# Kernel optimization log

Measured on AMD Instinct MI355X. Metric: run time of the kernel, lower is better.

Reference implementation:

```python
import jax, jax.numpy as jnp
import numpy as np

N_NODES = 50000
N_EDGES = 1250000
H_FEATS = 64


def setup_inputs() -> dict:
    key = jax.random.key(0)
    k1, k2, k3, k4, k5, k6, k7 = jax.random.split(key, 7)
    h = jax.random.normal(k1, (N_NODES, H_FEATS), dtype=jnp.float32)
    src = jax.random.randint(k2, (N_EDGES,), 0, N_NODES, dtype=jnp.int64)
    dst = jax.random.randint(k3, (N_EDGES,), 0, N_NODES, dtype=jnp.int64)
    # nn.Linear(2*h, h) and nn.Linear(h, 1); store weights as [in, out]
    s1 = 1.0 / np.sqrt(2 * H_FEATS)
    s2 = 1.0 / np.sqrt(H_FEATS)
    W1 = jax.random.uniform(k4, (2 * H_FEATS, H_FEATS), jnp.float32, -s1, s1)
    b1 = jax.random.uniform(k5, (H_FEATS,), jnp.float32, -s1, s1)
    W2 = jax.random.uniform(k6, (H_FEATS, 1), jnp.float32, -s2, s2)
    b2 = jax.random.uniform(k7, (1,), jnp.float32, -s2, s2)
    return {"h": h, "src": src, "dst": dst, "W1": W1, "b1": b1, "W2": W2, "b2": b2}


def reference(h, src, dst, W1, b1, W2, b2):
    # Gather per-edge endpoint features and concat: [E, 2*h_feats]
    he = jnp.concatenate([h[src], h[dst]], axis=1)
    hid = jax.nn.relu(he @ W1 + b1)          # [E, h_feats]
    score = (hid @ W2 + b2)[:, 0]            # [E]
    label = jnp.round(jax.nn.sigmoid(score))  # [E]
    return score, label
```

## Files before the change

kernel.cpp:

```cpp
#include <hip/hip_runtime.h>
#include <hip/hip_bf16.h>

#define H 64
#define NPB 64
#define EPB 128
#define FB_THRESH 0.015f

__device__ __forceinline__ unsigned short f2bf(float f) {
    unsigned u = __float_as_uint(f);
    unsigned r = (u + 0x7fffu + ((u >> 16) & 1u)) >> 16;
    return (unsigned short)r;
}
__device__ __forceinline__ float bf_lo(unsigned w) { return __uint_as_float(w << 16); }
__device__ __forceinline__ float bf_hi(unsigned w) { return __uint_as_float(w & 0xffff0000u); }

__global__ void __launch_bounds__(256)
node_proj_kernel(const float* __restrict__ h,
                 const float* __restrict__ W1,
                 float* __restrict__ A32,
                 float* __restrict__ B32,
                 unsigned short* __restrict__ Abf,
                 unsigned short* __restrict__ Bbf,
                 int n_nodes) {
    __shared__ float sh[NPB * H];
    const int t = threadIdx.x;
    const int c = t & 63;
    const int w = t >> 6;
    const int base = blockIdx.x * NPB;

    {
        const float4* hg = (const float4*)(h + (size_t)base * H);
        float4* shv = (float4*)sh;
#pragma unroll
        for (int i = 0; i < 4; ++i) {
            const int idx = t + i * 256;
            const int node = base + (idx >> 4);
            if (node < n_nodes) shv[idx] = hg[idx];
        }
    }

    float wA[64], wB[64];
#pragma unroll
    for (int k = 0; k < 64; ++k) {
        wA[k] = W1[k * H + c];
        wB[k] = W1[(k + 64) * H + c];
    }
    __syncthreads();

#pragma unroll 1
    for (int n0 = 0; n0 < 8; ++n0) {
        const int nl = w * 16 + n0 * 2;
        const int node = base + nl;
        if (node >= n_nodes) break;
        const bool two = (node + 1) < n_nodes;
        const float4* hr0 = (const float4*)(sh + nl * H);
        const float4* hr1 = (const float4*)(sh + (nl + 1) * H);
        float a0 = 0.f, b0 = 0.f, a1 = 0.f, b1acc = 0.f;
#pragma unroll
        for (int kk = 0; kk < 16; ++kk) {
            const float4 h0 = hr0[kk];
            const float4 h1 = hr1[kk];
            a0 = fmaf(h0.x, wA[4 * kk + 0], a0);
            a0 = fmaf(h0.y, wA[4 * kk + 1], a0);
            a0 = fmaf(h0.z, wA[4 * kk + 2], a0);
            a0 = fmaf(h0.w, wA[4 * kk + 3], a0);
            b0 = fmaf(h0.x, wB[4 * kk + 0], b0);
            b0 = fmaf(h0.y, wB[4 * kk + 1], b0);
            b0 = fmaf(h0.z, wB[4 * kk + 2], b0);
            b0 = fmaf(h0.w, wB[4 * kk + 3], b0);
            a1 = fmaf(h1.x, wA[4 * kk + 0], a1);
            a1 = fmaf(h1.y, wA[4 * kk + 1], a1);
            a1 = fmaf(h1.z, wA[4 * kk + 2], a1);
            a1 = fmaf(h1.w, wA[4 * kk + 3], a1);
            b1acc = fmaf(h1.x, wB[4 * kk + 0], b1acc);
            b1acc = fmaf(h1.y, wB[4 * kk + 1], b1acc);
            b1acc = fmaf(h1.z, wB[4 * kk + 2], b1acc);
            b1acc = fmaf(h1.w, wB[4 * kk + 3], b1acc);
        }
        A32[(size_t)node * H + c] = a0;
        B32[(size_t)node * H + c] = b0;
        Abf[(size_t)node * H + c] = f2bf(a0);
        Bbf[(size_t)node * H + c] = f2bf(b0);
        if (two) {
            A32[(size_t)(node + 1) * H + c] = a1;
            B32[(size_t)(node + 1) * H + c] = b1acc;
            Abf[(size_t)(node + 1) * H + c] = f2bf(a1);
            Bbf[(size_t)(node + 1) * H + c] = f2bf(b1acc);
        }
    }
}

__global__ void __launch_bounds__(256)
edge_score_kernel(const unsigned short* __restrict__ Abf,
                  const unsigned short* __restrict__ Bbf,
                  const float* __restrict__ A32,
                  const float* __restrict__ B32,
                  const int* __restrict__ src,
                  const int* __restrict__ dst,
                  const float* __restrict__ b1,
                  const float* __restrict__ W2,
                  const float* __restrict__ b2,
                  float* __restrict__ score_out,
                  float* __restrict__ label_out,
                  int n_edges) {
    const int t = threadIdx.x;
    const int sub = t & 15;
    const int group = t >> 4;

    const float4 b1v = ((const float4*)b1)[sub];
    const float4 w2v = ((const float4*)W2)[sub];
    const float b2s = b2[0];

    const int e0 = blockIdx.x * EPB + group;

    int ec[8], s[8], d[8];
#pragma unroll
    for (int i = 0; i < 8; ++i) {
        const int e = e0 + i * 16;
        ec[i] = e < n_edges ? e : (n_edges - 1);
    }
#pragma unroll
    for (int i = 0; i < 8; ++i) { s[i] = src[ec[i]]; d[i] = dst[ec[i]]; }

    uint2 av[8], cv[8];
#pragma unroll
    for (int i = 0; i < 8; ++i)
        av[i] = ((const uint2*)(Abf + (size_t)s[i] * H))[sub];
#pragma unroll
    for (int i = 0; i < 8; ++i)
        cv[i] = ((const uint2*)(Bbf + (size_t)d[i] * H))[sub];

#pragma unroll
    for (int i = 0; i < 8; ++i) {
        const float a0 = bf_lo(av[i].x), a1 = bf_hi(av[i].x);
        const float a2 = bf_lo(av[i].y), a3 = bf_hi(av[i].y);
        const float c0 = bf_lo(cv[i].x), c1 = bf_hi(cv[i].x);
        const float c2 = bf_lo(cv[i].y), c3 = bf_hi(cv[i].y);
        const float h0 = fmaxf(a0 + c0 + b1v.x, 0.f);
        const float h1 = fmaxf(a1 + c1 + b1v.y, 0.f);
        const float h2 = fmaxf(a2 + c2 + b1v.z, 0.f);
        const float h3 = fmaxf(a3 + c3 + b1v.w, 0.f);
        float p = h0 * w2v.x + h1 * w2v.y + h2 * w2v.z + h3 * w2v.w;
        p += __shfl_xor(p, 1);
        p += __shfl_xor(p, 2);
        p += __shfl_xor(p, 4);
        p += __shfl_xor(p, 8);
        float sc = p + b2s;

        if (fabsf(sc) < FB_THRESH) {
            const float4 a4 = ((const float4*)(A32 + (size_t)s[i] * H))[sub];
            const float4 c4 = ((const float4*)(B32 + (size_t)d[i] * H))[sub];
            const float g0 = fmaxf(a4.x + c4.x + b1v.x, 0.f);
            const float g1 = fmaxf(a4.y + c4.y + b1v.y, 0.f);
            const float g2 = fmaxf(a4.z + c4.z + b1v.z, 0.f);
            const float g3 = fmaxf(a4.w + c4.w + b1v.w, 0.f);
            float q = g0 * w2v.x + g1 * w2v.y + g2 * w2v.z + g3 * w2v.w;
            q += __shfl_xor(q, 1);
            q += __shfl_xor(q, 2);
            q += __shfl_xor(q, 4);
            q += __shfl_xor(q, 8);
            sc = q + b2s;
        }

        const int e = e0 + i * 16;
        if (sub == 0 && e < n_edges) {
            score_out[e] = sc;
            label_out[e] = sc > 0.f ? 1.f : 0.f;
        }
    }
}

extern "C" void kernel_launch(void* const* d_in, const int* in_sizes, int n_in,
                              void* d_out, int out_size, void* d_ws, size_t ws_size,
                              hipStream_t stream) {
    const float* h   = (const float*)d_in[0];
    const int*   src = (const int*)  d_in[1];
    const int*   dst = (const int*)  d_in[2];
    const float* W1  = (const float*)d_in[3];
    const float* b1  = (const float*)d_in[4];
    const float* W2  = (const float*)d_in[5];
    const float* b2  = (const float*)d_in[6];

    const int n_nodes = in_sizes[0] / H;
    const int n_edges = in_sizes[1];

    float* A32 = (float*)d_ws;
    float* B32 = A32 + (size_t)n_nodes * H;
    unsigned short* Abf = (unsigned short*)(B32 + (size_t)n_nodes * H);
    unsigned short* Bbf = Abf + (size_t)n_nodes * H;

    float* score_out = (float*)d_out;
    float* label_out = score_out + n_edges;

    {
        const int blocks = (n_nodes + NPB - 1) / NPB;
        node_proj_kernel<<<blocks, 256, 0, stream>>>(h, W1, A32, B32, Abf, Bbf,
                                                     n_nodes);
    }
    {
        const int blocks = (n_edges + EPB - 1) / EPB;
        edge_score_kernel<<<blocks, 256, 0, stream>>>(Abf, Bbf, A32, B32,
                                                      src, dst, b1, W2, b2,
                                                      score_out, label_out,
                                                      n_edges);
    }
}
```

Measured before the change: 147.0 us.

## Switch edge gather to fp16 with packed half2 math and 8-lane edge groups

```diff
diff --git a/kernel.cpp b/kernel.cpp
--- a/kernel.cpp
+++ b/kernel.cpp
@@ -3,24 +3,38 @@
 
 #define H 64
 #define NPB 64
-#define EPB 128
-#define FB_THRESH 0.015f
-
-__device__ __forceinline__ unsigned short f2bf(float f) {
-    unsigned u = __float_as_uint(f);
-    unsigned r = (u + 0x7fffu + ((u >> 16) & 1u)) >> 16;
-    return (unsigned short)r;
-}
-__device__ __forceinline__ float bf_lo(unsigned w) { return __uint_as_float(w << 16); }
-__device__ __forceinline__ float bf_hi(unsigned w) { return __uint_as_float(w & 0xffff0000u); }
+#define EPT 8
+#define FB_THRESH 0.008f
+
+typedef _Float16 half2_t __attribute__((ext_vector_type(2)));
+
+__device__ __forceinline__ half2_t h2relu(half2_t x) {
+#if defined(__has_builtin) && __has_builtin(__builtin_elementwise_max)
+    half2_t z = {(_Float16)0.f, (_Float16)0.f};
+    return __builtin_elementwise_max(x, z);
+#else
+    half2_t r;
+    r.x = x.x > (_Float16)0.f ? x.x : (_Float16)0.f;
+    r.y = x.y > (_Float16)0.f ? x.y : (_Float16)0.f;
+    return r;
+#endif
+}
+
+__device__ __forceinline__ float hdot2(half2_t a, half2_t b, float c) {
+#if defined(__has_builtin) && __has_builtin(__builtin_amdgcn_fdot2)
+    return __builtin_amdgcn_fdot2(a, b, c, false);
+#else
+    return c + (float)a.x * (float)b.x + (float)a.y * (float)b.y;
+#endif
+}
 
 __global__ void __launch_bounds__(256)
 node_proj_kernel(const float* __restrict__ h,
                  const float* __restrict__ W1,
                  float* __restrict__ A32,
                  float* __restrict__ B32,
-                 unsigned short* __restrict__ Abf,
-                 unsigned short* __restrict__ Bbf,
+                 _Float16* __restrict__ A16,
+                 _Float16* __restrict__ B16,
                  int n_nodes) {
     __shared__ float sh[NPB * H];
     const int t = threadIdx.x;
@@ -79,20 +93,20 @@
         }
         A32[(size_t)node * H + c] = a0;
         B32[(size_t)node * H + c] = b0;
-        Abf[(size_t)node * H + c] = f2bf(a0);
-        Bbf[(size_t)node * H + c] = f2bf(b0);
+        A16[(size_t)node * H + c] = (_Float16)a0;
+        B16[(size_t)node * H + c] = (_Float16)b0;
         if (two) {
             A32[(size_t)(node + 1) * H + c] = a1;
             B32[(size_t)(node + 1) * H + c] = b1acc;
-            Abf[(size_t)(node + 1) * H + c] = f2bf(a1);
-            Bbf[(size_t)(node + 1) * H + c] = f2bf(b1acc);
+            A16[(size_t)(node + 1) * H + c] = (_Float16)a1;
+            B16[(size_t)(node + 1) * H + c] = (_Float16)b1acc;
         }
     }
 }
 
 __global__ void __launch_bounds__(256)
-edge_score_kernel(const unsigned short* __restrict__ Abf,
-                  const unsigned short* __restrict__ Bbf,
+edge_score_kernel(const _Float16* __restrict__ A16,
+                  const _Float16* __restrict__ B16,
                   const float* __restrict__ A32,
                   const float* __restrict__ B32,
                   const int* __restrict__ src,
@@ -104,65 +118,79 @@
                   float* __restrict__ label_out,
                   int n_edges) {
     const int t = threadIdx.x;
-    const int sub = t & 15;
-    const int group = t >> 4;
-
-    const float4 b1v = ((const float4*)b1)[sub];
-    const float4 w2v = ((const float4*)W2)[sub];
+    const int sub = t & 7;
+    const int group = t >> 3;
+
+    const float4 b1lo = ((const float4*)b1)[sub * 2 + 0];
+    const float4 b1hi = ((const float4*)b1)[sub * 2 + 1];
+    const float4 w2lo = ((const float4*)W2)[sub * 2 + 0];
+    const float4 w2hi = ((const float4*)W2)[sub * 2 + 1];
+    half2_t b1h[4], w2h[4];
+    b1h[0] = (half2_t){(_Float16)b1lo.x, (_Float16)b1lo.y};
+    b1h[1] = (half2_t){(_Float16)b1lo.z, (_Float16)b1lo.w};
+    b1h[2] = (half2_t){(_Float16)b1hi.x, (_Float16)b1hi.y};
+    b1h[3] = (half2_t){(_Float16)b1hi.z, (_Float16)b1hi.w};
+    w2h[0] = (half2_t){(_Float16)w2lo.x, (_Float16)w2lo.y};
+    w2h[1] = (half2_t){(_Float16)w2lo.z, (_Float16)w2lo.w};
+    w2h[2] = (half2_t){(_Float16)w2hi.x, (_Float16)w2hi.y};
+    w2h[3] = (half2_t){(_Float16)w2hi.z, (_Float16)w2hi.w};
     const float b2s = b2[0];
 
-    const int e0 = blockIdx.x * EPB + group;
-
-    int ec[8], s[8], d[8];
-#pragma unroll
-    for (int i = 0; i < 8; ++i) {
-        const int e = e0 + i * 16;
+    const int e0 = blockIdx.x * (256 / 8 * EPT) + group;
+
+    int ec[EPT], s[EPT], d[EPT];
+#pragma unroll
+    for (int i = 0; i < EPT; ++i) {
+        const int e = e0 + i * 32;
         ec[i] = e < n_edges ? e : (n_edges - 1);
     }
 #pragma unroll
-    for (int i = 0; i < 8; ++i) { s[i] = src[ec[i]]; d[i] = dst[ec[i]]; }
-
-    uint2 av[8], cv[8];
-#pragma unroll
-    for (int i = 0; i < 8; ++i)
-        av[i] = ((const uint2*)(Abf + (size_t)s[i] * H))[sub];
-#pragma unroll
-    for (int i = 0; i < 8; ++i)
-        cv[i] = ((const uint2*)(Bbf + (size_t)d[i] * H))[sub];
-
-#pragma unroll
-    for (int i = 0; i < 8; ++i) {
-        const float a0 = bf_lo(av[i].x), a1 = bf_hi(av[i].x);
-        const float a2 = bf_lo(av[i].y), a3 = bf_hi(av[i].y);
-        const float c0 = bf_lo(cv[i].x), c1 = bf_hi(cv[i].x);
-        const float c2 = bf_lo(cv[i].y), c3 = bf_hi(cv[i].y);
-        const float h0 = fmaxf(a0 + c0 + b1v.x, 0.f);
-        const float h1 = fmaxf(a1 + c1 + b1v.y, 0.f);
-        const float h2 = fmaxf(a2 + c2 + b1v.z, 0.f);
-        const float h3 = fmaxf(a3 + c3 + b1v.w, 0.f);
-        float p = h0 * w2v.x + h1 * w2v.y + h2 * w2v.z + h3 * w2v.w;
+    for (int i = 0; i < EPT; ++i) { s[i] = src[ec[i]]; d[i] = dst[ec[i]]; }
+
+    float4 av[EPT], cv[EPT];
+#pragma unroll
+    for (int i = 0; i < EPT; ++i)
+        av[i] = ((const float4*)(A16 + (size_t)s[i] * H))[sub];
+#pragma unroll
+    for (int i = 0; i < EPT; ++i)
+        cv[i] = ((const float4*)(B16 + (size_t)d[i] * H))[sub];
+
+#pragma unroll
+    for (int i = 0; i < EPT; ++i) {
+        const half2_t* a2 = (const half2_t*)&av[i];
+        const half2_t* c2 = (const half2_t*)&cv[i];
+        float p = 0.f;
+#pragma unroll
+        for (int j = 0; j < 4; ++j) {
+            half2_t hj = h2relu(a2[j] + c2[j] + b1h[j]);
+            p = hdot2(hj, w2h[j], p);
+        }
         p += __shfl_xor(p, 1);
         p += __shfl_xor(p, 2);
         p += __shfl_xor(p, 4);
-        p += __shfl_xor(p, 8);
         float sc = p + b2s;
 
         if (fabsf(sc) < FB_THRESH) {
-            const float4 a4 = ((const float4*)(A32 + (size_t)s[i] * H))[sub];
-            const float4 c4 = ((const float4*)(B32 + (size_t)d[i] * H))[sub];
-            const float g0 = fmaxf(a4.x + c4.x + b1v.x, 0.f);
-            const float g1 = fmaxf(a4.y + c4.y + b1v.y, 0.f);
-            const float g2 = fmaxf(a4.z + c4.z + b1v.z, 0.f);
-            const float g3 = fmaxf(a4.w + c4.w + b1v.w, 0.f);
-            float q = g0 * w2v.x + g1 * w2v.y + g2 * w2v.z + g3 * w2v.w;
+            const float4 ra0 = ((const float4*)(A32 + (size_t)s[i] * H))[sub * 2 + 0];
+            const float4 ra1 = ((const float4*)(A32 + (size_t)s[i] * H))[sub * 2 + 1];
+            const float4 rb0 = ((const float4*)(B32 + (size_t)d[i] * H))[sub * 2 + 0];
+            const float4 rb1 = ((const float4*)(B32 + (size_t)d[i] * H))[sub * 2 + 1];
+            float q = 0.f;
+            q += fmaxf(ra0.x + rb0.x + b1lo.x, 0.f) * w2lo.x;
+            q += fmaxf(ra0.y + rb0.y + b1lo.y, 0.f) * w2lo.y;
+            q += fmaxf(ra0.z + rb0.z + b1lo.z, 0.f) * w2lo.z;
+            q += fmaxf(ra0.w + rb0.w + b1lo.w, 0.f) * w2lo.w;
+            q += fmaxf(ra1.x + rb1.x + b1hi.x, 0.f) * w2hi.x;
+            q += fmaxf(ra1.y + rb1.y + b1hi.y, 0.f) * w2hi.y;
+            q += fmaxf(ra1.z + rb1.z + b1hi.z, 0.f) * w2hi.z;
+            q += fmaxf(ra1.w + rb1.w + b1hi.w, 0.f) * w2hi.w;
             q += __shfl_xor(q, 1);
             q += __shfl_xor(q, 2);
             q += __shfl_xor(q, 4);
-            q += __shfl_xor(q, 8);
             sc = q + b2s;
         }
 
-        const int e = e0 + i * 16;
+        const int e = e0 + i * 32;
         if (sub == 0 && e < n_edges) {
             score_out[e] = sc;
             label_out[e] = sc > 0.f ? 1.f : 0.f;
@@ -186,20 +214,21 @@
 
     float* A32 = (float*)d_ws;
     float* B32 = A32 + (size_t)n_nodes * H;
-    unsigned short* Abf = (unsigned short*)(B32 + (size_t)n_nodes * H);
-    unsigned short* Bbf = Abf + (size_t)n_nodes * H;
+    _Float16* A16 = (_Float16*)(B32 + (size_t)n_nodes * H);
+    _Float16* B16 = A16 + (size_t)n_nodes * H;
 
     float* score_out = (float*)d_out;
     float* label_out = score_out + n_edges;
 
     {
         const int blocks = (n_nodes + NPB - 1) / NPB;
-        node_proj_kernel<<<blocks, 256, 0, stream>>>(h, W1, A32, B32, Abf, Bbf,
+        node_proj_kernel<<<blocks, 256, 0, stream>>>(h, W1, A32, B32, A16, B16,
                                                      n_nodes);
     }
     {
-        const int blocks = (n_edges + EPB - 1) / EPB;
-        edge_score_kernel<<<blocks, 256, 0, stream>>>(Abf, Bbf, A32, B32,
+        const int epb = 256 / 8 * EPT;
+        const int blocks = (n_edges + epb - 1) / epb;
+        edge_score_kernel<<<blocks, 256, 0, stream>>>(A16, B16, A32, B32,
                                                       src, dst, b1, W2, b2,
                                                       score_out, label_out,
                                                       n_edges);
```

Result: faster. 138.8 us, median of 2 (-5.6%).
